# Optimization experiments

Hardware: AMD Instinct MI355X
Metric: run time of the kernel (lower is better)

Reference implementation:

```python
import jax, jax.numpy as jnp
import numpy as np

N = 100_000   # nodes
D = 128       # feature dim (dim_in == dim_out, residual requires it)
E = 1_600_000 # edges
T = 4         # num_layers; edge_attr (hop distance) in 1..T


def setup_inputs() -> dict:
    key = jax.random.key(0)
    k0, k1, k2, k3, k4 = jax.random.split(key, 5)
    x = jax.random.normal(k0, (N, D), dtype=jnp.float32)
    edge_index = jax.random.randint(k1, (2, E), 0, N, dtype=jnp.int32)
    edge_attr = jax.random.randint(k2, (E,), 1, T + 1, dtype=jnp.int32)  # hop k in [1, T]
    W = jax.random.normal(k3, (T, D, D), dtype=jnp.float32) * (1.0 / np.sqrt(D))
    nu = jax.random.normal(k4, (T, T), dtype=jnp.float32) * 0.1  # nu[k-1, t]
    return {"x": x, "edge_index": edge_index, "edge_attr": edge_attr, "W": W, "nu": nu}


def _gcn_edge_coef(edge_index, mask, n):
    """Symmetric GCN normalization 1/sqrt(deg_src*deg_dst) restricted to masked edges."""
    src, dst = edge_index[0], edge_index[1]
    deg_s = jax.ops.segment_sum(mask, src, num_segments=n)
    deg_d = jax.ops.segment_sum(mask, dst, num_segments=n)
    inv = lambda d: jnp.where(d > 0, jax.lax.rsqrt(jnp.maximum(d, 1.0)), 0.0)
    return mask * inv(deg_s)[src] * inv(deg_d)[dst]  # [E]


def reference(x, edge_index, edge_attr, W, nu):
    n = x.shape[0]
    T_layers = nu.shape[1]
    src, dst = edge_index[0], edge_index[1]
    # Precompute per-hop normalized edge coefficients (A(k) masks as weights -> static shapes)
    coefs = [_gcn_edge_coef(edge_index, (edge_attr == k).astype(x.dtype), n)
             for k in range(1, T_layers + 1)]
    hist = [x]  # x_t history
    for t in range(T_layers):
        acc = jnp.zeros_like(x)
        for k in range(1, t + 2):  # k = 1 .. t+1
            h = hist[t + 1 - k] @ W[k - 1]                      # [N, D] linear
            msg = h[src] * coefs[k - 1][:, None]                # gather + weight [E, D]
            agg = jax.ops.segment_sum(msg, dst, num_segments=n) # scatter-sum [N, D]
            acc = acc + nu[k - 1, t] * agg
        xt = hist[t] + jax.nn.relu(acc)                         # residual + ReLU
        # F.normalize(p=2, dim=-1), eps=1e-12 (cfg.gnn.l2norm assumed True)
        xt = xt / jnp.maximum(jnp.linalg.norm(xt, axis=-1, keepdims=True), 1e-12)
        hist.append(xt)
    return hist[-1]
```

## Files before the change

kernel.cpp:

```cpp
#include <hip/hip_runtime.h>

#define DD 128
#define NP 128
#define EB 16384

typedef float4 f4;
typedef __attribute__((ext_vector_type(8))) short bf16x8;
typedef __attribute__((ext_vector_type(4))) float f32x4;

__device__ __forceinline__ short toBf(float f) {
    unsigned u = __float_as_uint(f);
    u += 0x7fff + ((u >> 16) & 1);
    return (short)(u >> 16);
}
__device__ __forceinline__ float bf2f(unsigned short u) {
    return __uint_as_float(((unsigned)u) << 16);
}


__global__ __launch_bounds__(1024) void kA(const int* __restrict__ ei, int E, int PSZ, int nbA,
                                           int* __restrict__ cntB_D, int* __restrict__ cntB_S) {
    __shared__ int hd[NP], hs[NP];
    int tid = threadIdx.x;
    if (tid < NP) { hd[tid] = 0; hs[tid] = 0; }
    __syncthreads();
    int base = blockIdx.x * EB;
    int lim = min(base + EB, E);
    for (int e = base + tid; e < lim; e += 1024) {
        int s = ei[e], d = ei[E + e];
        atomicAdd(&hs[s / PSZ], 1);
        atomicAdd(&hd[d / PSZ], 1);
    }
    __syncthreads();
    if (tid < NP) {
        cntB_D[tid * nbA + blockIdx.x] = hd[tid];
        cntB_S[tid * nbA + blockIdx.x] = hs[tid];
    }
}

__global__ __launch_bounds__(1024) void kB(int* __restrict__ cntB, int L, int nbA,
                                           int* __restrict__ partStart, int E) {
    __shared__ int sh[1024];
    int tid = threadIdx.x;
    int CH = (L + 1023) / 1024;
    int b0 = tid * CH, b1 = min(b0 + CH, L);
    int s = 0;
    for (int i = b0; i < b1; i++) s += cntB[i];
    sh[tid] = s; __syncthreads();
    for (int off = 1; off < 1024; off <<= 1) {
        int add = (tid >= off) ? sh[tid - off] : 0;
        __syncthreads(); sh[tid] += add; __syncthreads();
    }
    int run = (tid == 0) ? 0 : sh[tid - 1];
    for (int i = b0; i < b1; i++) {
        int v = cntB[i];
        cntB[i] = run;
        if (i % nbA == 0) partStart[i / nbA] = run;
        run += v;
    }
    if (tid == 0) partStart[NP] = E;
}

__global__ __launch_bounds__(1024) void kC(const int* __restrict__ ei, const int* __restrict__ ea,
                                           int E, int N, int T, int PSZ, int nbA,
                                           const int* __restrict__ cntB_D, const int* __restrict__ cntB_S,
                                           int2* __restrict__ binD, int* __restrict__ binS) {
    __shared__ int pd[NP], ps[NP];
    int tid = threadIdx.x, b = blockIdx.x;
    if (tid < NP) {
        pd[tid] = cntB_D[tid * nbA + b];
        ps[tid] = cntB_S[tid * nbA + b];
    }
    __syncthreads();
    int base = b * EB;
    int lim = min(base + EB, E);
    for (int e = base + tid; e < lim; e += 1024) {
        int s = ei[e], d = ei[E + e], k = ea[e] - 1;
        int dp = d / PSZ, sp = s / PSZ;
        int posD = atomicAdd(&pd[dp], 1);
        binD[posD] = make_int2((d - dp * PSZ) * T + k, (k << 26) | (k * N + s));
        int posS = atomicAdd(&ps[sp], 1);
        binS[posS] = (s - sp * PSZ) * T + k;
    }
}

__global__ __launch_bounds__(512) void kD(const int2* __restrict__ binD,
                                          const int* __restrict__ partStartD,
                                          int N, int T, int PSZ, int M, int E,
                                          int* __restrict__ rowptr, float* __restrict__ isdD2,
                                          int* __restrict__ ep) {
    __shared__ int cnt[4096];
    __shared__ int part[512];
    int p = blockIdx.x, tid = threadIdx.x;
    int nloc = PSZ * T;
    for (int i = tid; i < nloc; i += 512) cnt[i] = 0;
    __syncthreads();
    int b0 = partStartD[p], b1 = partStartD[p + 1];
    for (int e = b0 + tid; e < b1; e += 512) atomicAdd(&cnt[binD[e].x], 1);
    __syncthreads();
    int CH = (nloc + 511) / 512;
    int c0 = tid * CH, c1 = min(c0 + CH, nloc);
    int s = 0;
    for (int i = c0; i < c1; i++) s += cnt[i];
    part[tid] = s; __syncthreads();
    for (int off = 1; off < 512; off <<= 1) {
        int add = (tid >= off) ? part[tid - off] : 0;
        __syncthreads(); part[tid] += add; __syncthreads();
    }
    int run = ((tid == 0) ? 0 : part[tid - 1]) + b0;
    int gb_base = p * PSZ * T;
    for (int i = c0; i < c1; i++) {
        int v = cnt[i];
        cnt[i] = run;
        int gb = gb_base + i;
        if (gb < M) {
            rowptr[gb] = run;
            isdD2[gb] = rsqrtf((float)max(v, 1));
        }
        run += v;
    }
    __syncthreads();
    for (int e = b0 + tid; e < b1; e += 512) {
        int2 v = binD[e];
        int pos = atomicAdd(&cnt[v.x], 1);
        ep[pos] = v.y;
    }
    if (p == 0 && tid == 0) rowptr[M] = E;
}

__global__ __launch_bounds__(512) void kE(const int* __restrict__ binS,
                                          const int* __restrict__ partStartS,
                                          int N, int T, int PSZ, float* __restrict__ isdS) {
    __shared__ int cnt[4096];
    int p = blockIdx.x, tid = threadIdx.x;
    int nloc = PSZ * T;
    for (int i = tid; i < nloc; i += 512) cnt[i] = 0;
    __syncthreads();
    int b0 = partStartS[p], b1 = partStartS[p + 1];
    for (int e = b0 + tid; e < b1; e += 512) atomicAdd(&cnt[binS[e]], 1);
    __syncthreads();
    int s0 = p * PSZ;
    for (int i = tid; i < nloc; i += 512) {
        int sl = i / T, k = i - sl * T;
        int snode = s0 + sl;
        if (snode < N) isdS[k * N + snode] = rsqrtf((float)max(cnt[i], 1));
    }
}

__global__ void k_prepW(const float* __restrict__ W, ushort* __restrict__ WT, int tot) {
    int i = blockIdx.x * blockDim.x + threadIdx.x;
    if (i >= tot) return;
    int k = i >> 14, rem = i & 16383, j = rem >> 7, d = rem & 127;
    WT[i] = (ushort)toBf(W[(size_t)k * 16384 + (size_t)d * DD + j]);
}

__global__ void k_cvt(const float* __restrict__ x, ushort* __restrict__ xb, int n8) {
    int i = blockIdx.x * blockDim.x + threadIdx.x;
    if (i >= n8) return;
    const f4* q = (const f4*)(x + (size_t)i * 8);
    f4 lo = q[0], hi = q[1];
    bf16x8 r;
    r[0] = toBf(lo.x); r[1] = toBf(lo.y); r[2] = toBf(lo.z); r[3] = toBf(lo.w);
    r[4] = toBf(hi.x); r[5] = toBf(hi.y); r[6] = toBf(hi.z); r[7] = toBf(hi.w);
    *(bf16x8*)(xb + (size_t)i * 8) = r;
}


struct APtrs { const ushort* a0; const ushort* a1; const ushort* a2; const ushort* a3; };

__global__ __launch_bounds__(256) void k_gemm_batch(APtrs ap,
                                                    const ushort* __restrict__ WTb,
                                                    const float* __restrict__ iskb,
                                                    ushort* __restrict__ Hb, int N) {
    __shared__ ushort lW[128 * 128];
    int k0 = blockIdx.y;
    const ushort* A = (k0 == 0) ? ap.a0 : (k0 == 1) ? ap.a1 : (k0 == 2) ? ap.a2 : ap.a3;
    const ushort* WT = WTb + (size_t)k0 * DD * DD;
    const float* isk = iskb + (size_t)k0 * N;
    ushort* H = Hb + (size_t)k0 * N * DD;

    int tid = threadIdx.x;
#pragma unroll
    for (int i = 0; i < 8; i++) {
        int g = tid + i * 256;
        int row = g >> 4, slot = g & 15;
        bf16x8 v = *(const bf16x8*)(WT + row * DD + slot * 8);
        *(bf16x8*)(lW + row * DD + (slot ^ (row & 7)) * 8) = v;
    }
    __syncthreads();

    int wave = tid >> 6;
    int lane = tid & 63;
    int rlo = lane & 15;
    int khi = lane >> 4;
    int r0 = blockIdx.x * 256 + wave * 64;

    f32x4 acc[4][8];
#pragma unroll
    for (int s = 0; s < 4; s++)
#pragma unroll
        for (int j = 0; j < 8; j++) acc[s][j] = (f32x4){0.f, 0.f, 0.f, 0.f};

    int ca[4];
#pragma unroll
    for (int s = 0; s < 4; s++) {
        int r = r0 + s * 16 + rlo;
        ca[s] = r < N ? r : N - 1;
    }

#pragma unroll
    for (int kk = 0; kk < 4; kk++) {
        int d0 = kk * 32 + khi * 8;
        bf16x8 a[4];
#pragma unroll
        for (int s = 0; s < 4; s++)
            a[s] = *(const bf16x8*)(A + (size_t)ca[s] * DD + d0);
        int q = kk * 4 + khi;
#pragma unroll
        for (int cg = 0; cg < 8; cg++) {
            int row = cg * 16 + rlo;
            bf16x8 b = *(const bf16x8*)(lW + row * DD + (q ^ (rlo & 7)) * 8);
#pragma unroll
            for (int s = 0; s < 4; s++)
                acc[s][cg] = __builtin_amdgcn_mfma_f32_16x16x32_bf16(a[s], b, acc[s][cg], 0, 0, 0);
        }
    }

#pragma unroll
    for (int s = 0; s < 4; s++) {
#pragma unroll
        for (int r = 0; r < 4; r++) {
            int row = r0 + s * 16 + khi * 4 + r;
            if (row < N) {
                float sc = isk[row];
#pragma unroll
                for (int cg = 0; cg < 8; cg++)
                    H[(size_t)row * DD + cg * 16 + rlo] = (ushort)toBf(sc * acc[s][cg][r]);
            }
        }
    }
}


__device__ __forceinline__ float selw(float w0, float w1, float w2, float w3, int k) {
    float a = (k & 1) ? w1 : w0;
    float b = (k & 1) ? w3 : w2;
    return (k & 2) ? b : a;
}

__global__ __launch_bounds__(256) void k_agg_fin(
        const ushort* __restrict__ H,
        const int* __restrict__ ep,
        const int* __restrict__ rp,
        const float* __restrict__ isdD2,
        const float* __restrict__ nu, int t, int T, int nk,
        const ushort* __restrict__ hp,
        ushort* __restrict__ hnB,
        float* __restrict__ outF,
        int N) {
    int node = (blockIdx.x * blockDim.x + threadIdx.x) >> 5;
    if (node >= N) return;
    int lane = threadIdx.x & 31;
    int rbase = node * T;
    int b0 = rp[rbase], b1 = rp[rbase + nk];

    float w0 = nu[t] * isdD2[rbase];
    float w1 = (1 < nk) ? nu[T + t]     * isdD2[rbase + 1] : 0.f;
    float w2 = (2 < nk) ? nu[2 * T + t] * isdD2[rbase + 2] : 0.f;
    float w3 = (3 < nk) ? nu[3 * T + t] * isdD2[rbase + 3] : 0.f;

    const char* Hc = (const char*)H;
    unsigned lb = (unsigned)lane << 3;

    float sx = 0.f, sy = 0.f, sz = 0.f, sw = 0.f;
    int e = b0;

#define DEC(P, O, C) \
    O = ((((unsigned)(P)) & 0x3FFFFFFu) << 8) | lb; \
    C = selw(w0, w1, w2, w3, (P) >> 26);

#define ACC(G, C) { \
    float f0 = __uint_as_float((G).x << 16); \
    float f1 = __uint_as_float((G).x & 0xffff0000u); \
    float f2 = __uint_as_float((G).y << 16); \
    float f3 = __uint_as_float((G).y & 0xffff0000u); \
    sx = fmaf((C), f0, sx); sy = fmaf((C), f1, sy); \
    sz = fmaf((C), f2, sz); sw = fmaf((C), f3, sw); }

    for (; e + 7 < b1; e += 8) {
        int p0 = ep[e],     p1 = ep[e + 1], p2 = ep[e + 2], p3 = ep[e + 3];
        int p4 = ep[e + 4], p5 = ep[e + 5], p6 = ep[e + 6], p7 = ep[e + 7];
        unsigned o0, o1, o2, o3, o4, o5, o6, o7;
        float c0, c1, c2, c3, c4, c5, c6, c7;
        DEC(p0, o0, c0) DEC(p1, o1, c1) DEC(p2, o2, c2) DEC(p3, o3, c3)
        DEC(p4, o4, c4) DEC(p5, o5, c5) DEC(p6, o6, c6) DEC(p7, o7, c7)
        uint2 g0 = *(const uint2*)(Hc + o0);
        uint2 g1 = *(const uint2*)(Hc + o1);
        uint2 g2 = *(const uint2*)(Hc + o2);
        uint2 g3 = *(const uint2*)(Hc + o3);
        uint2 g4 = *(const uint2*)(Hc + o4);
        uint2 g5 = *(const uint2*)(Hc + o5);
        uint2 g6 = *(const uint2*)(Hc + o6);
        uint2 g7 = *(const uint2*)(Hc + o7);
        ACC(g0, c0) ACC(g1, c1) ACC(g2, c2) ACC(g3, c3)
        ACC(g4, c4) ACC(g5, c5) ACC(g6, c6) ACC(g7, c7)
    }
    if (e + 3 < b1) {
        int p0 = ep[e], p1 = ep[e + 1], p2 = ep[e + 2], p3 = ep[e + 3];
        unsigned o0, o1, o2, o3;
        float c0, c1, c2, c3;
        DEC(p0, o0, c0) DEC(p1, o1, c1) DEC(p2, o2, c2) DEC(p3, o3, c3)
        uint2 g0 = *(const uint2*)(Hc + o0);
        uint2 g1 = *(const uint2*)(Hc + o1);
        uint2 g2 = *(const uint2*)(Hc + o2);
        uint2 g3 = *(const uint2*)(Hc + o3);
        ACC(g0, c0) ACC(g1, c1) ACC(g2, c2) ACC(g3, c3)
        e += 4;
    }
    for (; e < b1; e++) {
        int p0 = ep[e];
        unsigned o0; float c0;
        DEC(p0, o0, c0)
        uint2 g0 = *(const uint2*)(Hc + o0);
        ACC(g0, c0)
    }
#undef DEC
#undef ACC

    unsigned nodeOff = ((unsigned)node << 8) | lb;
    uint2 hv = *(const uint2*)((const char*)hp + nodeOff);
    float vx = __uint_as_float(hv.x << 16)         + fmaxf(sx, 0.f);
    float vy = __uint_as_float(hv.x & 0xffff0000u) + fmaxf(sy, 0.f);
    float vz = __uint_as_float(hv.y << 16)         + fmaxf(sz, 0.f);
    float vw = __uint_as_float(hv.y & 0xffff0000u) + fmaxf(sw, 0.f);
    float ss = vx * vx + vy * vy + vz * vz + vw * vw;
#pragma unroll
    for (int off = 16; off; off >>= 1) ss += __shfl_xor(ss, off, 32);
    float inv = 1.f / fmaxf(sqrtf(ss), 1e-12f);
    vx *= inv; vy *= inv; vz *= inv; vw *= inv;
    if (outF) {
        f4 o; o.x = vx; o.y = vy; o.z = vz; o.w = vw;
        *(f4*)((char*)outF + (((size_t)node << 9) | ((size_t)lane << 4))) = o;
    } else {
        uint lo = ((unsigned)(unsigned short)toBf(vx)) | (((unsigned)(unsigned short)toBf(vy)) << 16);
        uint hi = ((unsigned)(unsigned short)toBf(vz)) | (((unsigned)(unsigned short)toBf(vw)) << 16);
        uint2 ob; ob.x = lo; ob.y = hi;
        *(uint2*)((char*)hnB + nodeOff) = ob;
    }
}


extern "C" void kernel_launch(void* const* d_in, const int* in_sizes, int n_in,
                              void* d_out, int out_size, void* d_ws, size_t ws_size,
                              hipStream_t stream) {
    const float* x  = (const float*)d_in[0];
    const int*   ei = (const int*)d_in[1];
    const int*   ea = (const int*)d_in[2];
    const float* W  = (const float*)d_in[3];
    const float* nu = (const float*)d_in[4];
    float* out = (float*)d_out;

    int N = in_sizes[0] / DD;
    int E = in_sizes[1] / 2;
    int T = in_sizes[3] / (DD * DD);
    int M = T * N;
    size_t ND = (size_t)N * DD;

    int PSZ = (N + NP - 1) / NP;
    if (PSZ * T > 4096) return;
    int nbA = (E + EB - 1) / EB;

    float*  isdS  = (float*)d_ws;
    float*  isdD2 = isdS + M;
    ushort* xb    = (ushort*)(isdD2 + M);
    ushort* h1b   = xb + ND;
    ushort* h2b   = h1b + ND;
    ushort* h3b   = h2b + ND;
    ushort* Hb    = h3b + ND;
    ushort* WT    = Hb + (size_t)T * ND;
    int* rowptr   = (int*)(WT + (size_t)T * DD * DD);
    int* ep       = rowptr + M + 1;
    int2* binD       = (int2*)Hb;
    int*  binS       = (int*)(binD + E);
    int*  cntB_D     = binS + E;
    int*  cntB_S     = cntB_D + NP * nbA;
    int*  partStartD = cntB_S + NP * nbA;
    int*  partStartS = partStartD + NP + 1;

    size_t req = sizeof(float) * 2 * (size_t)M
               + sizeof(ushort) * ((size_t)(4 + T) * ND + (size_t)T * DD * DD)
               + sizeof(int) * ((size_t)M + 1 + (size_t)E + 64);
    if (ws_size < req) return;
    size_t scratch = sizeof(int) * (3 * (size_t)E + 2 * (size_t)NP * nbA + 2 * (NP + 1));
    if (scratch > sizeof(ushort) * (size_t)T * ND) return;

    kA<<<nbA, 1024, 0, stream>>>(ei, E, PSZ, nbA, cntB_D, cntB_S);
    kB<<<1, 1024, 0, stream>>>(cntB_D, NP * nbA, nbA, partStartD, E);
    kB<<<1, 1024, 0, stream>>>(cntB_S, NP * nbA, nbA, partStartS, E);
    kC<<<nbA, 1024, 0, stream>>>(ei, ea, E, N, T, PSZ, nbA, cntB_D, cntB_S, binD, binS);
    kD<<<NP, 512, 0, stream>>>(binD, partStartD, N, T, PSZ, M, E, rowptr, isdD2, ep);
    kE<<<NP, 512, 0, stream>>>(binS, partStartS, N, T, PSZ, isdS);
    k_prepW<<<(T * DD * DD + 255) / 256, 256, 0, stream>>>(W, WT, T * DD * DD);
    k_cvt<<<((int)(ND / 8) + 255) / 256, 256, 0, stream>>>(x, xb, (int)(ND / 8));

    const ushort* histB[4] = {xb, h1b, h2b, h3b};

    int nodeBlocks = ((size_t)N * 32 + 255) / 256;
    int gemmBlocks = (N + 255) / 256;

    for (int t = 0; t < T; t++) {
        APtrs ap;
        ap.a0 = histB[t];
        ap.a1 = (t >= 1) ? histB[t - 1] : histB[0];
        ap.a2 = (t >= 2) ? histB[t - 2] : histB[0];
        ap.a3 = (t >= 3) ? histB[t - 3] : histB[0];
        dim3 grid(gemmBlocks, t + 1);
        k_gemm_batch<<<grid, 256, 0, stream>>>(ap, WT, isdS, Hb, N);

        bool lastL = (t == T - 1);
        k_agg_fin<<<nodeBlocks, 256, 0, stream>>>(Hb, ep, rowptr, isdD2,
                                                  nu, t, T, t + 1, histB[t],
                                                  lastL ? nullptr : (ushort*)histB[t + 1],
                                                  lastL ? out : nullptr, N);
    }
}
```

Before: 458.0 us.

## Replace two-level partitioned CSR build with global-atomic count, scan, place

The CSR preprocessing used to bin edges into partitions with shared-memory atomics before building per-partition CSR. It now counts degrees directly with global atomics, runs a three-kernel device-wide scan, and places edges into final positions with global atomics. The intermediate binD/binS buffers and a pass over them are gone, and isdS/isdD2 are computed in the scan kernel while reusing the count arrays in place. In exchange the count and place steps rely on contended global atomics, and edge order within each row is now nondeterministic.

```diff
diff --git a/kernel.cpp b/kernel.cpp
--- a/kernel.cpp
+++ b/kernel.cpp
@@ -1,8 +1,7 @@
 #include <hip/hip_runtime.h>
 
 #define DD 128
-#define NP 128
-#define EB 16384
+#define SCH 4096
 
 typedef float4 f4;
 typedef __attribute__((ext_vector_type(8))) short bf16x8;
@@ -18,132 +17,95 @@
 }
 
 
-__global__ __launch_bounds__(1024) void kA(const int* __restrict__ ei, int E, int PSZ, int nbA,
-                                           int* __restrict__ cntB_D, int* __restrict__ cntB_S) {
-    __shared__ int hd[NP], hs[NP];
-    int tid = threadIdx.x;
-    if (tid < NP) { hd[tid] = 0; hs[tid] = 0; }
-    __syncthreads();
-    int base = blockIdx.x * EB;
-    int lim = min(base + EB, E);
-    for (int e = base + tid; e < lim; e += 1024) {
-        int s = ei[e], d = ei[E + e];
-        atomicAdd(&hs[s / PSZ], 1);
-        atomicAdd(&hd[d / PSZ], 1);
-    }
-    __syncthreads();
-    if (tid < NP) {
-        cntB_D[tid * nbA + blockIdx.x] = hd[tid];
-        cntB_S[tid * nbA + blockIdx.x] = hs[tid];
-    }
-}
-
-__global__ __launch_bounds__(1024) void kB(int* __restrict__ cntB, int L, int nbA,
-                                           int* __restrict__ partStart, int E) {
+__global__ __launch_bounds__(1024) void kZero(int* __restrict__ p, int n) {
+    int i = blockIdx.x * 1024 + threadIdx.x;
+    if (i < n) p[i] = 0;
+}
+
+__global__ __launch_bounds__(256) void kCount(const int* __restrict__ ei, const int* __restrict__ ea,
+                                              int E, int N, int T,
+                                              int* __restrict__ cntD, int* __restrict__ cntS) {
+    int stride = gridDim.x * 256;
+    for (int e = blockIdx.x * 256 + threadIdx.x; e < E; e += stride) {
+        int s = ei[e], d = ei[E + e], k = ea[e] - 1;
+        atomicAdd(&cntD[d * T + k], 1);
+        atomicAdd(&cntS[k * N + s], 1);
+    }
+}
+
+__global__ __launch_bounds__(1024) void kS1(const int* __restrict__ cntD, int M, int* __restrict__ bsum) {
+    __shared__ int sh[1024];
+    int b = blockIdx.x, tid = threadIdx.x;
+    int i0 = b * SCH + tid * 4;
+    int s = 0;
+#pragma unroll
+    for (int j = 0; j < 4; j++) { int i = i0 + j; if (i < M) s += cntD[i]; }
+    sh[tid] = s; __syncthreads();
+    for (int off = 512; off; off >>= 1) {
+        if (tid < off) sh[tid] += sh[tid + off];
+        __syncthreads();
+    }
+    if (tid == 0) bsum[b] = sh[0];
+}
+
+__global__ __launch_bounds__(1024) void kS2(int* __restrict__ bsum, int nb) {
     __shared__ int sh[1024];
     int tid = threadIdx.x;
-    int CH = (L + 1023) / 1024;
-    int b0 = tid * CH, b1 = min(b0 + CH, L);
+    sh[tid] = (tid < nb) ? bsum[tid] : 0;
+    __syncthreads();
+    for (int off = 1; off < 1024; off <<= 1) {
+        int add = (tid >= off) ? sh[tid - off] : 0;
+        __syncthreads(); sh[tid] += add; __syncthreads();
+    }
+    if (tid < nb) bsum[tid] = (tid == 0) ? 0 : sh[tid - 1];
+}
+
+__global__ __launch_bounds__(1024) void kS3(int* __restrict__ cntD_isdD2,
+                                            int* __restrict__ cntS_isdS,
+                                            const int* __restrict__ bsum, int M, int E,
+                                            int* __restrict__ rowptr, int* __restrict__ ofs) {
+    __shared__ int sh[1024];
+    int b = blockIdx.x, tid = threadIdx.x;
+    int i0 = b * SCH + tid * 4;
+    int c[4];
     int s = 0;
-    for (int i = b0; i < b1; i++) s += cntB[i];
+#pragma unroll
+    for (int j = 0; j < 4; j++) {
+        int i = i0 + j;
+        c[j] = (i < M) ? cntD_isdD2[i] : 0;
+        s += c[j];
+    }
     sh[tid] = s; __syncthreads();
     for (int off = 1; off < 1024; off <<= 1) {
         int add = (tid >= off) ? sh[tid - off] : 0;
         __syncthreads(); sh[tid] += add; __syncthreads();
     }
-    int run = (tid == 0) ? 0 : sh[tid - 1];
-    for (int i = b0; i < b1; i++) {
-        int v = cntB[i];
-        cntB[i] = run;
-        if (i % nbA == 0) partStart[i / nbA] = run;
-        run += v;
-    }
-    if (tid == 0) partStart[NP] = E;
-}
-
-__global__ __launch_bounds__(1024) void kC(const int* __restrict__ ei, const int* __restrict__ ea,
-                                           int E, int N, int T, int PSZ, int nbA,
-                                           const int* __restrict__ cntB_D, const int* __restrict__ cntB_S,
-                                           int2* __restrict__ binD, int* __restrict__ binS) {
-    __shared__ int pd[NP], ps[NP];
-    int tid = threadIdx.x, b = blockIdx.x;
-    if (tid < NP) {
-        pd[tid] = cntB_D[tid * nbA + b];
-        ps[tid] = cntB_S[tid * nbA + b];
-    }
-    __syncthreads();
-    int base = b * EB;
-    int lim = min(base + EB, E);
-    for (int e = base + tid; e < lim; e += 1024) {
+    int run = bsum[b] + sh[tid] - s;
+    float* isdD2 = (float*)cntD_isdD2;
+    float* isdS  = (float*)cntS_isdS;
+#pragma unroll
+    for (int j = 0; j < 4; j++) {
+        int i = i0 + j;
+        if (i < M) {
+            rowptr[i] = run;
+            ofs[i] = run;
+            int cs = cntS_isdS[i];
+            isdD2[i] = rsqrtf((float)max(c[j], 1));
+            isdS[i]  = rsqrtf((float)max(cs, 1));
+            run += c[j];
+        }
+    }
+    if (b == 0 && tid == 0) rowptr[M] = E;
+}
+
+__global__ __launch_bounds__(256) void kPlace(const int* __restrict__ ei, const int* __restrict__ ea,
+                                              int E, int N, int T,
+                                              int* __restrict__ ofs, int* __restrict__ ep) {
+    int stride = gridDim.x * 256;
+    for (int e = blockIdx.x * 256 + threadIdx.x; e < E; e += stride) {
         int s = ei[e], d = ei[E + e], k = ea[e] - 1;
-        int dp = d / PSZ, sp = s / PSZ;
-        int posD = atomicAdd(&pd[dp], 1);
-        binD[posD] = make_int2((d - dp * PSZ) * T + k, (k << 26) | (k * N + s));
-        int posS = atomicAdd(&ps[sp], 1);
-        binS[posS] = (s - sp * PSZ) * T + k;
-    }
-}
-
-__global__ __launch_bounds__(512) void kD(const int2* __restrict__ binD,
-                                          const int* __restrict__ partStartD,
-                                          int N, int T, int PSZ, int M, int E,
-                                          int* __restrict__ rowptr, float* __restrict__ isdD2,
-                                          int* __restrict__ ep) {
-    __shared__ int cnt[4096];
-    __shared__ int part[512];
-    int p = blockIdx.x, tid = threadIdx.x;
-    int nloc = PSZ * T;
-    for (int i = tid; i < nloc; i += 512) cnt[i] = 0;
-    __syncthreads();
-    int b0 = partStartD[p], b1 = partStartD[p + 1];
-    for (int e = b0 + tid; e < b1; e += 512) atomicAdd(&cnt[binD[e].x], 1);
-    __syncthreads();
-    int CH = (nloc + 511) / 512;
-    int c0 = tid * CH, c1 = min(c0 + CH, nloc);
-    int s = 0;
-    for (int i = c0; i < c1; i++) s += cnt[i];
-    part[tid] = s; __syncthreads();
-    for (int off = 1; off < 512; off <<= 1) {
-        int add = (tid >= off) ? part[tid - off] : 0;
-        __syncthreads(); part[tid] += add; __syncthreads();
-    }
-    int run = ((tid == 0) ? 0 : part[tid - 1]) + b0;
-    int gb_base = p * PSZ * T;
-    for (int i = c0; i < c1; i++) {
-        int v = cnt[i];
-        cnt[i] = run;
-        int gb = gb_base + i;
-        if (gb < M) {
-            rowptr[gb] = run;
-            isdD2[gb] = rsqrtf((float)max(v, 1));
-        }
-        run += v;
-    }
-    __syncthreads();
-    for (int e = b0 + tid; e < b1; e += 512) {
-        int2 v = binD[e];
-        int pos = atomicAdd(&cnt[v.x], 1);
-        ep[pos] = v.y;
-    }
-    if (p == 0 && tid == 0) rowptr[M] = E;
-}
-
-__global__ __launch_bounds__(512) void kE(const int* __restrict__ binS,
-                                          const int* __restrict__ partStartS,
-                                          int N, int T, int PSZ, float* __restrict__ isdS) {
-    __shared__ int cnt[4096];
-    int p = blockIdx.x, tid = threadIdx.x;
-    int nloc = PSZ * T;
-    for (int i = tid; i < nloc; i += 512) cnt[i] = 0;
-    __syncthreads();
-    int b0 = partStartS[p], b1 = partStartS[p + 1];
-    for (int e = b0 + tid; e < b1; e += 512) atomicAdd(&cnt[binS[e]], 1);
-    __syncthreads();
-    int s0 = p * PSZ;
-    for (int i = tid; i < nloc; i += 512) {
-        int sl = i / T, k = i - sl * T;
-        int snode = s0 + sl;
-        if (snode < N) isdS[k * N + snode] = rsqrtf((float)max(cnt[i], 1));
+        int pos = atomicAdd(&ofs[d * T + k], 1);
+        ep[pos] = (k << 26) | (k * N + s);
     }
 }
 
@@ -366,9 +328,8 @@
     int M = T * N;
     size_t ND = (size_t)N * DD;
 
-    int PSZ = (N + NP - 1) / NP;
-    if (PSZ * T > 4096) return;
-    int nbA = (E + EB - 1) / EB;
+    int nbS = (M + SCH - 1) / SCH;
+    if (nbS > 1024) return;
 
     float*  isdS  = (float*)d_ws;
     float*  isdD2 = isdS + M;
@@ -380,26 +341,22 @@
     ushort* WT    = Hb + (size_t)T * ND;
     int* rowptr   = (int*)(WT + (size_t)T * DD * DD);
     int* ep       = rowptr + M + 1;
-    int2* binD       = (int2*)Hb;
-    int*  binS       = (int*)(binD + E);
-    int*  cntB_D     = binS + E;
-    int*  cntB_S     = cntB_D + NP * nbA;
-    int*  partStartD = cntB_S + NP * nbA;
-    int*  partStartS = partStartD + NP + 1;
+    int* ofs  = (int*)Hb;
+    int* bsum = ofs + M;
 
     size_t req = sizeof(float) * 2 * (size_t)M
                + sizeof(ushort) * ((size_t)(4 + T) * ND + (size_t)T * DD * DD)
                + sizeof(int) * ((size_t)M + 1 + (size_t)E + 64);
     if (ws_size < req) return;
-    size_t scratch = sizeof(int) * (3 * (size_t)E + 2 * (size_t)NP * nbA + 2 * (NP + 1));
+    size_t scratch = sizeof(int) * ((size_t)M + nbS + 64);
     if (scratch > sizeof(ushort) * (size_t)T * ND) return;
 
-    kA<<<nbA, 1024, 0, stream>>>(ei, E, PSZ, nbA, cntB_D, cntB_S);
-    kB<<<1, 1024, 0, stream>>>(cntB_D, NP * nbA, nbA, partStartD, E);
-    kB<<<1, 1024, 0, stream>>>(cntB_S, NP * nbA, nbA, partStartS, E);
-    kC<<<nbA, 1024, 0, stream>>>(ei, ea, E, N, T, PSZ, nbA, cntB_D, cntB_S, binD, binS);
-    kD<<<NP, 512, 0, stream>>>(binD, partStartD, N, T, PSZ, M, E, rowptr, isdD2, ep);
-    kE<<<NP, 512, 0, stream>>>(binS, partStartS, N, T, PSZ, isdS);
+    kZero<<<(2 * M + 1023) / 1024, 1024, 0, stream>>>((int*)isdS, 2 * M);
+    kCount<<<2048, 256, 0, stream>>>(ei, ea, E, N, T, (int*)isdD2, (int*)isdS);
+    kS1<<<nbS, 1024, 0, stream>>>((int*)isdD2, M, bsum);
+    kS2<<<1, 1024, 0, stream>>>(bsum, nbS);
+    kS3<<<nbS, 1024, 0, stream>>>((int*)isdD2, (int*)isdS, bsum, M, E, rowptr, ofs);
+    kPlace<<<2048, 256, 0, stream>>>(ei, ea, E, N, T, ofs, ep);
     k_prepW<<<(T * DD * DD + 255) / 256, 256, 0, stream>>>(W, WT, T * DD * DD);
     k_cvt<<<((int)(ND / 8) + 255) / 256, 256, 0, stream>>>(x, xb, (int)(ND / 8));
 
```

After: 605.6 us. 32.2% more time.

## Double graph-build partitions and merge prefix-scan and binning kernels into single launches

Applied to the files above, without the earlier changes.

Raises the partition count from 128 to 256 and halves the per-block edge chunk, so the CSR build phases use more blocks on the many-CU GPU. The two single-block scan launches merge into one two-block launch, and the dst-binning and src-degree kernels merge into one grid so they run concurrently. This cuts launch count and idle CUs in the preprocessing stage. The scan kernel now scans twice as many counters per block, which could lengthen that serial step.

```diff
diff --git a/kernel.cpp b/kernel.cpp
--- a/kernel.cpp
+++ b/kernel.cpp
@@ -1,8 +1,8 @@
 #include <hip/hip_runtime.h>
 
 #define DD 128
-#define NP 128
-#define EB 16384
+#define NP 256
+#define EB 8192
 
 typedef float4 f4;
 typedef __attribute__((ext_vector_type(8))) short bf16x8;
@@ -38,8 +38,12 @@
     }
 }
 
-__global__ __launch_bounds__(1024) void kB(int* __restrict__ cntB, int L, int nbA,
-                                           int* __restrict__ partStart, int E) {
+__global__ __launch_bounds__(1024) void kB(int* __restrict__ cntB_D, int* __restrict__ cntB_S,
+                                           int L, int nbA,
+                                           int* __restrict__ partStartD, int* __restrict__ partStartS,
+                                           int E) {
+    int* cntB = (blockIdx.x == 0) ? cntB_D : cntB_S;
+    int* partStart = (blockIdx.x == 0) ? partStartD : partStartS;
     __shared__ int sh[1024];
     int tid = threadIdx.x;
     int CH = (L + 1023) / 1024;
@@ -84,66 +88,63 @@
     }
 }
 
-__global__ __launch_bounds__(512) void kD(const int2* __restrict__ binD,
-                                          const int* __restrict__ partStartD,
-                                          int N, int T, int PSZ, int M, int E,
-                                          int* __restrict__ rowptr, float* __restrict__ isdD2,
-                                          int* __restrict__ ep) {
+__global__ __launch_bounds__(512) void kDE(const int2* __restrict__ binD,
+                                           const int* __restrict__ binS,
+                                           const int* __restrict__ partStartD,
+                                           const int* __restrict__ partStartS,
+                                           int N, int T, int PSZ, int M, int E,
+                                           int* __restrict__ rowptr, float* __restrict__ isdD2,
+                                           int* __restrict__ ep, float* __restrict__ isdS) {
     __shared__ int cnt[4096];
     __shared__ int part[512];
-    int p = blockIdx.x, tid = threadIdx.x;
+    int b = blockIdx.x, tid = threadIdx.x;
     int nloc = PSZ * T;
     for (int i = tid; i < nloc; i += 512) cnt[i] = 0;
     __syncthreads();
-    int b0 = partStartD[p], b1 = partStartD[p + 1];
-    for (int e = b0 + tid; e < b1; e += 512) atomicAdd(&cnt[binD[e].x], 1);
-    __syncthreads();
-    int CH = (nloc + 511) / 512;
-    int c0 = tid * CH, c1 = min(c0 + CH, nloc);
-    int s = 0;
-    for (int i = c0; i < c1; i++) s += cnt[i];
-    part[tid] = s; __syncthreads();
-    for (int off = 1; off < 512; off <<= 1) {
-        int add = (tid >= off) ? part[tid - off] : 0;
-        __syncthreads(); part[tid] += add; __syncthreads();
-    }
-    int run = ((tid == 0) ? 0 : part[tid - 1]) + b0;
-    int gb_base = p * PSZ * T;
-    for (int i = c0; i < c1; i++) {
-        int v = cnt[i];
-        cnt[i] = run;
-        int gb = gb_base + i;
-        if (gb < M) {
-            rowptr[gb] = run;
-            isdD2[gb] = rsqrtf((float)max(v, 1));
-        }
-        run += v;
-    }
-    __syncthreads();
-    for (int e = b0 + tid; e < b1; e += 512) {
-        int2 v = binD[e];
-        int pos = atomicAdd(&cnt[v.x], 1);
-        ep[pos] = v.y;
-    }
-    if (p == 0 && tid == 0) rowptr[M] = E;
-}
-
-__global__ __launch_bounds__(512) void kE(const int* __restrict__ binS,
-                                          const int* __restrict__ partStartS,
-                                          int N, int T, int PSZ, float* __restrict__ isdS) {
-    __shared__ int cnt[4096];
-    int p = blockIdx.x, tid = threadIdx.x;
-    int nloc = PSZ * T;
-    for (int i = tid; i < nloc; i += 512) cnt[i] = 0;
-    __syncthreads();
-    int b0 = partStartS[p], b1 = partStartS[p + 1];
-    for (int e = b0 + tid; e < b1; e += 512) atomicAdd(&cnt[binS[e]], 1);
-    __syncthreads();
-    int s0 = p * PSZ;
-    for (int i = tid; i < nloc; i += 512) {
-        int sl = i / T, k = i - sl * T;
-        int snode = s0 + sl;
-        if (snode < N) isdS[k * N + snode] = rsqrtf((float)max(cnt[i], 1));
+    if (b < NP) {
+        int p = b;
+        int b0 = partStartD[p], b1 = partStartD[p + 1];
+        for (int e = b0 + tid; e < b1; e += 512) atomicAdd(&cnt[binD[e].x], 1);
+        __syncthreads();
+        int CH = (nloc + 511) / 512;
+        int c0 = tid * CH, c1 = min(c0 + CH, nloc);
+        int s = 0;
+        for (int i = c0; i < c1; i++) s += cnt[i];
+        part[tid] = s; __syncthreads();
+        for (int off = 1; off < 512; off <<= 1) {
+            int add = (tid >= off) ? part[tid - off] : 0;
+            __syncthreads(); part[tid] += add; __syncthreads();
+        }
+        int run = ((tid == 0) ? 0 : part[tid - 1]) + b0;
+        int gb_base = p * PSZ * T;
+        for (int i = c0; i < c1; i++) {
+            int v = cnt[i];
+            cnt[i] = run;
+            int gb = gb_base + i;
+            if (gb < M) {
+                rowptr[gb] = run;
+                isdD2[gb] = rsqrtf((float)max(v, 1));
+            }
+            run += v;
+        }
+        __syncthreads();
+        for (int e = b0 + tid; e < b1; e += 512) {
+            int2 v = binD[e];
+            int pos = atomicAdd(&cnt[v.x], 1);
+            ep[pos] = v.y;
+        }
+        if (p == 0 && tid == 0) rowptr[M] = E;
+    } else {
+        int p = b - NP;
+        int b0 = partStartS[p], b1 = partStartS[p + 1];
+        for (int e = b0 + tid; e < b1; e += 512) atomicAdd(&cnt[binS[e]], 1);
+        __syncthreads();
+        int s0 = p * PSZ;
+        for (int i = tid; i < nloc; i += 512) {
+            int sl = i / T, k = i - sl * T;
+            int snode = s0 + sl;
+            if (snode < N) isdS[k * N + snode] = rsqrtf((float)max(cnt[i], 1));
+        }
     }
 }
 
@@ -395,11 +396,10 @@
     if (scratch > sizeof(ushort) * (size_t)T * ND) return;
 
     kA<<<nbA, 1024, 0, stream>>>(ei, E, PSZ, nbA, cntB_D, cntB_S);
-    kB<<<1, 1024, 0, stream>>>(cntB_D, NP * nbA, nbA, partStartD, E);
-    kB<<<1, 1024, 0, stream>>>(cntB_S, NP * nbA, nbA, partStartS, E);
+    kB<<<2, 1024, 0, stream>>>(cntB_D, cntB_S, NP * nbA, nbA, partStartD, partStartS, E);
     kC<<<nbA, 1024, 0, stream>>>(ei, ea, E, N, T, PSZ, nbA, cntB_D, cntB_S, binD, binS);
-    kD<<<NP, 512, 0, stream>>>(binD, partStartD, N, T, PSZ, M, E, rowptr, isdD2, ep);
-    kE<<<NP, 512, 0, stream>>>(binS, partStartS, N, T, PSZ, isdS);
+    kDE<<<2 * NP, 512, 0, stream>>>(binD, binS, partStartD, partStartS,
+                                    N, T, PSZ, M, E, rowptr, isdD2, ep, isdS);
     k_prepW<<<(T * DD * DD + 255) / 256, 256, 0, stream>>>(W, WT, T * DD * DD);
     k_cvt<<<((int)(ND / 8) + 255) / 256, 256, 0, stream>>>(x, xb, (int)(ND / 8));
 
```

Result: slower. 480.9 us (+5.0%).
